# Optimization experiments

Hardware: AMD Instinct MI355X
Metric: run time of the kernel (lower is better)

## Reference

```python
import jax, jax.numpy as jnp
import numpy as np

N, D, E, EDGE_DIM = 8192, 64, 262144, 4


def setup_inputs() -> dict:
    key = jax.random.key(0)
    k1, k2, k3, k4, k5, k6 = jax.random.split(key, 6)
    mag = jax.random.uniform(k1, (N, D), dtype=jnp.float32)
    phase = jax.random.normal(k2, (N, D), dtype=jnp.float32)
    edge_index = jax.random.randint(k3, (2, E), 0, N, dtype=jnp.int64)
    edge_attr = jax.random.normal(k4, (E, EDGE_DIM), dtype=jnp.float32)
    # nn.Linear(edge_dim, hidden_dim): weight [hidden_dim, edge_dim], bias [hidden_dim]
    bound = 1.0 / np.sqrt(EDGE_DIM)
    W = jax.random.uniform(k5, (D, EDGE_DIM), minval=-bound, maxval=bound, dtype=jnp.float32)
    b = jax.random.uniform(k6, (D,), minval=-bound, maxval=bound, dtype=jnp.float32)
    return {"mag": mag, "phase": phase, "edge_index": edge_index,
            "edge_attr": edge_attr, "W": W, "b": b}


def reference(mag, phase, edge_index, edge_attr, W, b):
    # score_ij = sum_d mag_i[d]*mag_j[d]*cos(phase_i[d]-phase_j[d])
    # Via cos(a-b) = cos a cos b + sin a sin b -> two [N,D]@[D,N] matmuls,
    # avoiding the O(N^2 D) intermediate while computing identical math.
    c = mag * jnp.cos(phase)  # [N, D]
    s = mag * jnp.sin(phase)  # [N, D]
    scores = c @ c.T + s @ s.T  # [N, N]
    # edge bias: edge_bias[src, dst] = sum_h Linear(edge_attr)[e, h]
    edge_scores = (edge_attr @ W.T + b).sum(axis=-1)  # [E]
    bias = jnp.zeros((mag.shape[0], mag.shape[0]), dtype=scores.dtype)
    bias = bias.at[edge_index[0], edge_index[1]].set(edge_scores)
    scores = scores + bias
    attn = jax.nn.softmax(scores, axis=1)  # [N, N]
    new_mag = attn @ mag  # [N, D]
    new_phase = attn @ phase  # [N, D]
    return new_mag, new_phase
```

## Files before the change

### kernel.cpp

```cpp
#include <hip/hip_runtime.h>
#include <hip/hip_bf16.h>
#include <cstdint>

#define N_NODES 8192
#define DDIM    64
#define DX      128
#define NEDGE   262144
#define BR      128
#define BC      64
#define SPLITS  8
#define TILES   (N_NODES / BC / SPLITS)
#define RCAP    64
#define MSHIFT  66.0f

typedef float f32x16 __attribute__((ext_vector_type(16)));
typedef short short8 __attribute__((ext_vector_type(8)));
typedef short short4v __attribute__((ext_vector_type(4)));

__device__ __forceinline__ short f2bf(float f) {
    union { float f; uint32_t u; } v; v.f = f;
    uint32_t u = v.u;
    uint32_t r = (u + 0x7FFFu + ((u >> 16) & 1u)) >> 16;
    return (short)r;
}
__device__ __forceinline__ float bf2f(short s) {
    union { uint32_t u; float f; } v;
    v.u = ((uint32_t)(uint16_t)s) << 16;
    return v.f;
}
__device__ __forceinline__ unsigned cvtpk_bf16(float lo, float hi) {
    unsigned r;
    asm("v_cvt_pk_bf16_f32 %0, %1, %2" : "=v"(r) : "v"(lo), "v"(hi));
    return r;
}
__device__ __forceinline__ void gload_lds16(const short* g, short* l) {
    __builtin_amdgcn_global_load_lds(
        (const __attribute__((address_space(1))) unsigned int*)g,
        (__attribute__((address_space(3))) unsigned int*)l, 16, 0, 0);
}

__global__ __launch_bounds__(256) void cpa_prep_all(
    const float* __restrict__ mag, const float* __restrict__ phase,
    const int* __restrict__ ei, const float* __restrict__ ea,
    const float* __restrict__ W, const float* __restrict__ b,
    short* __restrict__ Xbf, short* __restrict__ Ybt,
    short* __restrict__ esb, int* __restrict__ cnt,
    int* __restrict__ keys) {
    __shared__ short tile[64][65];
    __shared__ float wsb[5];
    const int blk = blockIdx.x;
    const int tid = threadIdx.x;
    if (blk < 512) {
        int idx4 = blk * 256 + tid;
        int i  = idx4 >> 4;
        int dq = (idx4 & 15) << 2;
        float4 m4 = *(const float4*)(mag   + (size_t)i * 64 + dq);
        float4 p4 = *(const float4*)(phase + (size_t)i * 64 + dq);
        short4v c4, s4;
        c4[0] = f2bf(m4.x * __cosf(p4.x)); s4[0] = f2bf(m4.x * __sinf(p4.x));
        c4[1] = f2bf(m4.y * __cosf(p4.y)); s4[1] = f2bf(m4.y * __sinf(p4.y));
        c4[2] = f2bf(m4.z * __cosf(p4.z)); s4[2] = f2bf(m4.z * __sinf(p4.z));
        c4[3] = f2bf(m4.w * __cosf(p4.w)); s4[3] = f2bf(m4.w * __sinf(p4.w));
        *(short4v*)(Xbf + (size_t)i * DX + dq)      = c4;
        *(short4v*)(Xbf + (size_t)i * DX + 64 + dq) = s4;
    } else if (blk < 768) {
        int bb = blk - 512;
        int bi = bb >> 1;
        int bc = bb & 1;
        int i0 = bi * 64;
        const float* src = bc ? phase : mag;
        for (int itr = 0; itr < 16; ++itr) {
            int idx = tid + itr * 256;
            int ii = idx >> 6, cc = idx & 63;
            tile[ii][cc] = f2bf(src[(size_t)(i0 + ii) * 64 + cc]);
        }
        __syncthreads();
        for (int itr = 0; itr < 16; ++itr) {
            int idx = tid + itr * 256;
            int cc = idx >> 6, ii = idx & 63;
            int jp = (ii & 51) | ((ii & 4) << 1) | ((ii & 8) >> 1);
            Ybt[(size_t)(bc * 64 + cc) * N_NODES + i0 + jp] = tile[ii][cc];
        }
    } else {
        if (tid < 64) {
            float w0 = W[tid * 4 + 0], w1 = W[tid * 4 + 1];
            float w2 = W[tid * 4 + 2], w3 = W[tid * 4 + 3];
            float bb = b[tid];
            #pragma unroll
            for (int o = 32; o > 0; o >>= 1) {
                w0 += __shfl_down(w0, o);
                w1 += __shfl_down(w1, o);
                w2 += __shfl_down(w2, o);
                w3 += __shfl_down(w3, o);
                bb += __shfl_down(bb, o);
            }
            if (tid == 0) { wsb[0] = w0; wsb[1] = w1; wsb[2] = w2; wsb[3] = w3; wsb[4] = bb; }
        }
        __syncthreads();
        int e = (blk - 768) * 256 + tid;
        float4 a = *(const float4*)(ea + (size_t)e * 4);
        esb[e] = f2bf(__expf(a.x * wsb[0] + a.y * wsb[1] + a.z * wsb[2] + a.w * wsb[3] + wsb[4]));
        int src = ei[e];
        int dst = ei[NEDGE + e];
        int pos = atomicAdd(&cnt[src], 1);
        if (pos < RCAP) keys[src * RCAP + pos] = (dst << 18) | e;
    }
}

__global__ __launch_bounds__(256) void cpa_sortrows(const int* __restrict__ cnt,
                                                    int* __restrict__ keys) {
    const int wv   = threadIdx.x >> 6;
    const int lane = threadIdx.x & 63;
    #pragma unroll
    for (int rr = 0; rr < 4; ++rr) {
        int row  = blockIdx.x * 16 + wv * 4 + rr;
        int len  = min(cnt[row], RCAP);
        int base = row * RCAP;
        int v = (lane < len) ? keys[base + lane] : 0x7FFFFFFF;

        #pragma unroll
        for (int k = 2; k <= 64; k <<= 1) {
            #pragma unroll
            for (int j = k >> 1; j >= 1; j >>= 1) {
                int p = __shfl_xor(v, j);
                bool asc = (lane & k) == 0;
                bool low = (lane & j) == 0;
                v = (low == asc) ? min(v, p) : max(v, p);
            }
        }
        int nxt = __shfl_down(v, 1);
        bool dead = (lane + 1 < len) && ((v >> 18) == (nxt >> 18));
        if (lane < len) keys[base + lane] = v | (dead ? 0x80000000 : 0);
    }
}

__global__ __launch_bounds__(512, 4) void cpa_flash(
    const short* __restrict__ Xbf, const short* __restrict__ Ybt,
    const short* __restrict__ esb, const int* __restrict__ keys,
    const int* __restrict__ cnt,
    float* __restrict__ lsplit, short* __restrict__ Opart)
{
    __shared__ short XjT[2][64][128];
    __shared__ short Yt[2][128][64];
    __shared__ unsigned swp[4][2][2][64][4];

    const int tid  = threadIdx.x;
    const int lane = tid & 63;
    const int w    = tid >> 6;
    const int l31  = lane & 31;
    const int lh   = lane >> 5;
    const int ig   = w >> 1;
    const int jg   = w & 1;

    const int split = blockIdx.x;
    const int ib    = blockIdx.y;
    const int i0 = ib * BR;
    const int jstart = split * (N_NODES / SPLITS);

    short8 xi[8];
    #pragma unroll
    for (int kf = 0; kf < 8; ++kf)
        xi[kf] = *(const short8*)(Xbf + (size_t)(i0 + ig * 32 + l31) * DX + kf * 16 + lh * 8);

    const int xr0 = w * 8 + (lane >> 4);
    const int xc  = lane & 15;
    const int xo0 = (xc ^ (xr0 & 15)) << 3;
    const int xr1 = xr0 + 4;
    const int xo1 = (xc ^ (xr1 & 15)) << 3;
    const int yr  = w * 16 + (lane >> 3);
    const int yo  = ((lane & 7) ^ (yr & 7)) << 3;
    const int yr2 = yr + 8;
    const int yo2 = ((lane & 7) ^ (yr2 & 7)) << 3;

    gload_lds16(Xbf + (size_t)(jstart + xr0) * DX + xo0, &XjT[0][w * 8][0]);
    gload_lds16(Xbf + (size_t)(jstart + xr1) * DX + xo1, &XjT[0][w * 8 + 4][0]);
    gload_lds16(Ybt + (size_t)yr * N_NODES + jstart + yo,   &Yt[0][w * 16][0]);
    gload_lds16(Ybt + (size_t)yr2 * N_NODES + jstart + yo2, &Yt[0][w * 16 + 8][0]);

    const int myrow = i0 + ig * 32 + l31;
    const int base  = myrow * RCAP;
    const int len   = min(cnt[myrow], RCAP);
    int lo = 0, hi = len;
    while (lo < hi) {
        int mid = (lo + hi) >> 1;
        int d = (keys[base + mid] >> 18) & 0x1FFF;
        if (d < jstart) lo = mid + 1; else hi = mid;
    }
    int cur  = base + lo;
    int rend = base + len;
    int kcur = 0;
    if (cur < rend) kcur = keys[cur];

    f32x16 O0, O1;
    float lacc = 0.f;
    #pragma unroll
    for (int r = 0; r < 16; ++r) { O0[r] = 0.f; O1[r] = 0.f; }

    for (int tt = 0; tt < TILES; ++tt) {
        const int j0 = jstart + tt * BC;
        const int bb = tt & 1;

        __syncthreads();

        if (tt + 1 < TILES) {
            gload_lds16(Xbf + (size_t)((j0 + BC) + xr0) * DX + xo0, &XjT[bb ^ 1][w * 8][0]);
            gload_lds16(Xbf + (size_t)((j0 + BC) + xr1) * DX + xo1, &XjT[bb ^ 1][w * 8 + 4][0]);
            gload_lds16(Ybt + (size_t)yr * N_NODES + (j0 + BC) + yo,   &Yt[bb ^ 1][w * 16][0]);
            gload_lds16(Ybt + (size_t)yr2 * N_NODES + (j0 + BC) + yo2, &Yt[bb ^ 1][w * 16 + 8][0]);
        }
        __builtin_amdgcn_sched_barrier(0);

        const int rr_ = jg * 32 + l31;
        f32x16 S;
        #pragma unroll
        for (int r = 0; r < 16; ++r) S[r] = 0.f;
        __builtin_amdgcn_s_setprio(1);
        #pragma unroll
        for (int kf = 0; kf < 8; ++kf) {
            short8 af = *(const short8*)&XjT[bb][rr_][((kf * 2 + lh) ^ (rr_ & 15)) << 3];
            S = __builtin_amdgcn_mfma_f32_32x32x16_bf16(af, xi[kf], S, 0, 0, 0);
        }
        __builtin_amdgcn_s_setprio(0);

        f32x16 p;
        #pragma unroll
        for (int r = 0; r < 16; ++r) p[r] = __expf(S[r] - MSHIFT);

        {
            const int wlo  = j0 + jg * 32;
            const int wend = wlo + 32;
            while (cur < rend) {
                int dst = (kcur >> 18) & 0x1FFF;
                if (dst >= wend) break;
                int kk = kcur;
                ++cur;
                if (cur < rend) kcur = keys[cur];
                int jl = dst - wlo;
                if (kk >= 0 && jl >= 0 && ((jl >> 2) & 1) == lh) {
                    float m = bf2f(esb[kk & 0x3FFFF]);
                    int sel = (jl & 3) | ((jl >> 3) << 2);
                    #pragma unroll
                    for (int r = 0; r < 16; ++r)
                        if (r == sel) p[r] *= m;
                }
            }
        }

        #pragma unroll
        for (int r = 0; r < 16; ++r) lacc += p[r];

        union FU { unsigned u[4]; short8 s; int4 v; };
        FU F0, F1;
        F0.u[0] = cvtpk_bf16(p[0], p[1]);   F0.u[1] = cvtpk_bf16(p[2], p[3]);
        F0.u[2] = cvtpk_bf16(p[4], p[5]);   F0.u[3] = cvtpk_bf16(p[6], p[7]);
        F1.u[0] = cvtpk_bf16(p[8], p[9]);   F1.u[1] = cvtpk_bf16(p[10], p[11]);
        F1.u[2] = cvtpk_bf16(p[12], p[13]); F1.u[3] = cvtpk_bf16(p[14], p[15]);

        *(int4*)&swp[ig][jg][0][lane][0] = F0.v;
        *(int4*)&swp[ig][jg][1][lane][0] = F1.v;

        const int fA = jg * 64 + l31;
        const int fB = fA + 32;
        __builtin_amdgcn_s_setprio(1);
        #pragma unroll
        for (int sl = 0; sl < 2; ++sl) {
            short8 ao = sl ? F1.s : F0.s;
            const int co_o = jg * 4 + sl * 2 + lh;
            short8 b0o = *(const short8*)&Yt[bb][fA][(co_o ^ (fA & 7)) << 3];
            short8 b1o = *(const short8*)&Yt[bb][fB][(co_o ^ (fB & 7)) << 3];
            O0 = __builtin_amdgcn_mfma_f32_32x32x16_bf16(ao, b0o, O0, 0, 0, 0);
            O1 = __builtin_amdgcn_mfma_f32_32x32x16_bf16(ao, b1o, O1, 0, 0, 0);
        }
        __builtin_amdgcn_s_setprio(0);

        asm volatile("s_waitcnt lgkmcnt(0)" ::: "memory");
        __builtin_amdgcn_s_barrier();
        __builtin_amdgcn_sched_barrier(0);

        __builtin_amdgcn_s_setprio(1);
        #pragma unroll
        for (int sl = 0; sl < 2; ++sl) {
            short8 at = *(const short8*)&swp[ig][jg ^ 1][sl][lane][0];
            const int co_t = (jg ^ 1) * 4 + sl * 2 + lh;
            short8 b0t = *(const short8*)&Yt[bb][fA][(co_t ^ (fA & 7)) << 3];
            short8 b1t = *(const short8*)&Yt[bb][fB][(co_t ^ (fB & 7)) << 3];
            O0 = __builtin_amdgcn_mfma_f32_32x32x16_bf16(at, b0t, O0, 0, 0, 0);
            O1 = __builtin_amdgcn_mfma_f32_32x32x16_bf16(at, b1t, O1, 0, 0, 0);
        }
        __builtin_amdgcn_s_setprio(0);
    }

    lacc += __shfl_xor(lacc, 32);
    __syncthreads();
    float* lmbuf = (float*)&swp[0][0][0][0][0];
    if (jg == 1 && lane < 32) lmbuf[ig * 32 + l31] = lacc;
    __syncthreads();
    if (jg == 0 && lane < 32)
        lsplit[(size_t)split * N_NODES + i0 + ig * 32 + l31] = lacc + lmbuf[ig * 32 + l31];

    #pragma unroll
    for (int r = 0; r < 16; ++r) {
        int row = ig * 32 + 4 * lh + (r & 3) + 8 * (r >> 2);
        size_t base2 = ((size_t)split * N_NODES + i0 + row) * DX;
        Opart[base2 + jg * 64 + l31]      = f2bf(O0[r]);
        Opart[base2 + jg * 64 + 32 + l31] = f2bf(O1[r]);
    }
}

__global__ __launch_bounds__(256) void cpa_merge(const float* __restrict__ lsplit,
                                                 const short* __restrict__ Opart,
                                                 float* __restrict__ out) {
    int gid = blockIdx.x * 256 + threadIdx.x;
    int i  = gid >> 4;
    int c8 = (gid & 15) << 3;
    float den = 0.f;
    float num[8];
    #pragma unroll
    for (int q = 0; q < 8; ++q) num[q] = 0.f;
    #pragma unroll
    for (int s = 0; s < SPLITS; ++s) {
        den += lsplit[(size_t)s * N_NODES + i];
        short8 v = *(const short8*)(Opart + ((size_t)s * N_NODES + i) * DX + c8);
        #pragma unroll
        for (int q = 0; q < 8; ++q) num[q] += bf2f(v[q]);
    }
    float inv = 1.0f / den;
    float4 o0, o1;
    o0.x = num[0] * inv; o0.y = num[1] * inv; o0.z = num[2] * inv; o0.w = num[3] * inv;
    o1.x = num[4] * inv; o1.y = num[5] * inv; o1.z = num[6] * inv; o1.w = num[7] * inv;
    float* dst = (c8 < 64) ? (out + (size_t)i * 64 + c8)
                           : (out + (size_t)N_NODES * 64 + (size_t)i * 64 + (c8 - 64));
    *(float4*)dst = o0;
    *(float4*)(dst + 4) = o1;
}

extern "C" void kernel_launch(void* const* d_in, const int* in_sizes, int n_in,
                              void* d_out, int out_size, void* d_ws, size_t ws_size,
                              hipStream_t stream)
{
    const float* mag   = (const float*)d_in[0];
    const float* phase = (const float*)d_in[1];
    const int*   ei    = (const int*)d_in[2];
    const float* ea    = (const float*)d_in[3];
    const float* W     = (const float*)d_in[4];
    const float* b     = (const float*)d_in[5];
    float* out = (float*)d_out;

    char* ws = (char*)d_ws;
    short* Xbf    = (short*)(ws + 0);
    short* Ybt    = (short*)(ws + 2097152);
    short* esb    = (short*)(ws + 4194304);
    int*   cnt    = (int*)  (ws + 4718592);
    int*   keys   = (int*)  (ws + 5242880);
    float* lsplit = (float*)(ws + 7373056);
    short* Opart  = (short*)(ws + 7635200);

    (void)hipMemsetAsync(cnt, 0, N_NODES * sizeof(int), stream);
    cpa_prep_all<<<512 + 256 + NEDGE / 256, 256, 0, stream>>>(mag, phase, ei, ea, W, b,
                                                              Xbf, Ybt, esb, cnt, keys);
    cpa_sortrows<<<N_NODES / 16, 256, 0, stream>>>(cnt, keys);
    cpa_flash<<<dim3(SPLITS, N_NODES / BR), 512, 0, stream>>>(Xbf, Ybt, esb, keys, cnt,
                                                              lsplit, Opart);
    cpa_merge<<<N_NODES * 16 / 256, 256, 0, stream>>>(lsplit, Opart, out);
}
```

Measured before the change: 150.6 us.

## Fuse split merge into flash kernel via last-block semaphore; one row per wave in sort

```diff
diff --git a/kernel.cpp b/kernel.cpp
--- a/kernel.cpp
+++ b/kernel.cpp
@@ -109,36 +109,33 @@
 
 __global__ __launch_bounds__(256) void cpa_sortrows(const int* __restrict__ cnt,
                                                     int* __restrict__ keys) {
-    const int wv   = threadIdx.x >> 6;
-    const int lane = threadIdx.x & 63;
+    int row  = blockIdx.x * 4 + (threadIdx.x >> 6);
+    int lane = threadIdx.x & 63;
+    int len  = min(cnt[row], RCAP);
+    int base = row * RCAP;
+    int v = (lane < len) ? keys[base + lane] : 0x7FFFFFFF;
+
     #pragma unroll
-    for (int rr = 0; rr < 4; ++rr) {
-        int row  = blockIdx.x * 16 + wv * 4 + rr;
-        int len  = min(cnt[row], RCAP);
-        int base = row * RCAP;
-        int v = (lane < len) ? keys[base + lane] : 0x7FFFFFFF;
-
-        #pragma unroll
-        for (int k = 2; k <= 64; k <<= 1) {
-            #pragma unroll
-            for (int j = k >> 1; j >= 1; j >>= 1) {
-                int p = __shfl_xor(v, j);
-                bool asc = (lane & k) == 0;
-                bool low = (lane & j) == 0;
-                v = (low == asc) ? min(v, p) : max(v, p);
-            }
-        }
-        int nxt = __shfl_down(v, 1);
-        bool dead = (lane + 1 < len) && ((v >> 18) == (nxt >> 18));
-        if (lane < len) keys[base + lane] = v | (dead ? 0x80000000 : 0);
-    }
+    for (int k = 2; k <= 64; k <<= 1) {
+        #pragma unroll
+        for (int j = k >> 1; j >= 1; j >>= 1) {
+            int p = __shfl_xor(v, j);
+            bool asc = (lane & k) == 0;
+            bool low = (lane & j) == 0;
+            v = (low == asc) ? min(v, p) : max(v, p);
+        }
+    }
+    int nxt = __shfl_down(v, 1);
+    bool dead = (lane + 1 < len) && ((v >> 18) == (nxt >> 18));
+    if (lane < len) keys[base + lane] = v | (dead ? 0x80000000 : 0);
 }
 
 __global__ __launch_bounds__(512, 4) void cpa_flash(
     const short* __restrict__ Xbf, const short* __restrict__ Ybt,
     const short* __restrict__ esb, const int* __restrict__ keys,
-    const int* __restrict__ cnt,
-    float* __restrict__ lsplit, short* __restrict__ Opart)
+    const int* __restrict__ cnt, int* __restrict__ sems,
+    float* __restrict__ lsplit, short* __restrict__ Opart,
+    float* __restrict__ out)
 {
     __shared__ short XjT[2][64][128];
     __shared__ short Yt[2][128][64];
@@ -305,33 +302,40 @@
         Opart[base2 + jg * 64 + l31]      = f2bf(O0[r]);
         Opart[base2 + jg * 64 + 32 + l31] = f2bf(O1[r]);
     }
-}
-
-__global__ __launch_bounds__(256) void cpa_merge(const float* __restrict__ lsplit,
-                                                 const short* __restrict__ Opart,
-                                                 float* __restrict__ out) {
-    int gid = blockIdx.x * 256 + threadIdx.x;
-    int i  = gid >> 4;
-    int c8 = (gid & 15) << 3;
-    float den = 0.f;
-    float num[8];
-    #pragma unroll
-    for (int q = 0; q < 8; ++q) num[q] = 0.f;
-    #pragma unroll
-    for (int s = 0; s < SPLITS; ++s) {
-        den += lsplit[(size_t)s * N_NODES + i];
-        short8 v = *(const short8*)(Opart + ((size_t)s * N_NODES + i) * DX + c8);
-        #pragma unroll
-        for (int q = 0; q < 8; ++q) num[q] += bf2f(v[q]);
-    }
-    float inv = 1.0f / den;
-    float4 o0, o1;
-    o0.x = num[0] * inv; o0.y = num[1] * inv; o0.z = num[2] * inv; o0.w = num[3] * inv;
-    o1.x = num[4] * inv; o1.y = num[5] * inv; o1.z = num[6] * inv; o1.w = num[7] * inv;
-    float* dst = (c8 < 64) ? (out + (size_t)i * 64 + c8)
-                           : (out + (size_t)N_NODES * 64 + (size_t)i * 64 + (c8 - 64));
-    *(float4*)dst = o0;
-    *(float4*)(dst + 4) = o1;
+
+    __threadfence();
+    __syncthreads();
+    volatile int* flg = ((volatile int*)swp) + 256;
+    if (tid == 0) *flg = atomicAdd(&sems[ib], 1);
+    __syncthreads();
+    if (*flg == 7) {
+        __threadfence();
+        #pragma unroll
+        for (int it = 0; it < 4; ++it) {
+            int u = it * 512 + tid;
+            int i = i0 + (u >> 4);
+            int c8 = (u & 15) << 3;
+            float den = 0.f;
+            float num[8];
+            #pragma unroll
+            for (int q = 0; q < 8; ++q) num[q] = 0.f;
+            #pragma unroll
+            for (int s = 0; s < SPLITS; ++s) {
+                den += lsplit[(size_t)s * N_NODES + i];
+                short8 v = *(const short8*)(Opart + ((size_t)s * N_NODES + i) * DX + c8);
+                #pragma unroll
+                for (int q = 0; q < 8; ++q) num[q] += bf2f(v[q]);
+            }
+            float inv = 1.0f / den;
+            float4 o0, o1;
+            o0.x = num[0] * inv; o0.y = num[1] * inv; o0.z = num[2] * inv; o0.w = num[3] * inv;
+            o1.x = num[4] * inv; o1.y = num[5] * inv; o1.z = num[6] * inv; o1.w = num[7] * inv;
+            float* dst = (c8 < 64) ? (out + (size_t)i * 64 + c8)
+                                   : (out + (size_t)N_NODES * 64 + (size_t)i * 64 + (c8 - 64));
+            *(float4*)dst = o0;
+            *(float4*)(dst + 4) = o1;
+        }
+    }
 }
 
 extern "C" void kernel_launch(void* const* d_in, const int* in_sizes, int n_in,
@@ -351,15 +355,15 @@
     short* Ybt    = (short*)(ws + 2097152);
     short* esb    = (short*)(ws + 4194304);
     int*   cnt    = (int*)  (ws + 4718592);
+    int*   sems   = (int*)  (ws + 4751360);
     int*   keys   = (int*)  (ws + 5242880);
     float* lsplit = (float*)(ws + 7373056);
     short* Opart  = (short*)(ws + 7635200);
 
-    (void)hipMemsetAsync(cnt, 0, N_NODES * sizeof(int), stream);
+    (void)hipMemsetAsync(cnt, 0, 33024, stream);
     cpa_prep_all<<<512 + 256 + NEDGE / 256, 256, 0, stream>>>(mag, phase, ei, ea, W, b,
                                                               Xbf, Ybt, esb, cnt, keys);
-    cpa_sortrows<<<N_NODES / 16, 256, 0, stream>>>(cnt, keys);
+    cpa_sortrows<<<N_NODES / 4, 256, 0, stream>>>(cnt, keys);
     cpa_flash<<<dim3(SPLITS, N_NODES / BR), 512, 0, stream>>>(Xbf, Ybt, esb, keys, cnt,
-                                                              lsplit, Opart);
-    cpa_merge<<<N_NODES * 16 / 256, 256, 0, stream>>>(lsplit, Opart, out);
-}
+                                                              sems, lsplit, Opart, out);
+}
```

After: 311.1 us. +106.6%, slower.
